# Kernel tuning notes

Measured on AMD Instinct MI355X. Metric: run time of the kernel, lower is better.

The kernel has to match this reference:

```python
import jax, jax.numpy as jnp
import numpy as np

N = 8192
D_IN = 512
HID = 1024
EMB = 64
N_EFF = 2
N_CLASSES = 16
MARGIN = 0.01


def setup_inputs() -> dict:
    key = jax.random.key(0)
    ks = jax.random.split(key, 10)
    data = jax.random.normal(ks[0], (N, D_IN), dtype=jnp.float32)
    labels = jax.random.randint(ks[1], (N,), 0, N_CLASSES).astype(jnp.float32)
    x = jnp.concatenate([labels[:, None], data], axis=1)  # [N, 1+D_IN]

    def lin(k, fan_in, fan_out):
        return jax.random.normal(k, (fan_in, fan_out), dtype=jnp.float32) / np.sqrt(fan_in)

    return {
        "x": x,
        "W1": lin(ks[2], D_IN, HID), "b1": jnp.zeros((HID,), jnp.float32),
        "W2": lin(ks[3], HID, EMB), "b2": jnp.zeros((EMB,), jnp.float32),
        "W3": lin(ks[4], EMB, HID), "b3": jnp.zeros((HID,), jnp.float32),
        "W4": lin(ks[5], HID, D_IN), "b4": jnp.zeros((D_IN,), jnp.float32),
    }


def reference(x, W1, b1, W2, b2, W3, b3, W4, b4):
    labels = x[:, 0]
    data = x[:, 1:]

    # encoder / decoder (tanh MLP autoencoder)
    embedding = jnp.tanh(data @ W1 + b1) @ W2 + b2          # [N, EMB]
    decoded = jnp.tanh(embedding @ W3 + b3) @ W4 + b4       # [N, D_IN]

    conserved = embedding[:, N_EFF:]                        # [N, C]
    n_conserved = conserved.shape[1]

    # labels.expand + unique(return_inverse) on row-replicated labels is
    # equivalent to comparing the labels directly.
    lbl = labels.astype(jnp.int32)
    Y = lbl[:, None] != lbl[None, :]                        # [N, N] bool

    # D_mean[i,j] = mean_d (c_i - c_j)^2, via Gram-matrix algebra (one pass,
    # no [N,N,C] intermediate).
    sq = jnp.sum(conserved * conserved, axis=1)             # [N]
    gram = conserved @ conserved.T                          # [N, N]
    D_mean = jnp.maximum(sq[:, None] + sq[None, :] - 2.0 * gram, 0.0) / n_conserved

    Yf = Y.astype(D_mean.dtype)
    n_diff = jnp.sum(Yf)
    C_sim = jnp.sum(Yf * D_mean) / (n_diff + 1.0)
    C_diff = jnp.sum((1.0 - Yf) * jnp.maximum(0.0, MARGIN - D_mean)) / (
        (D_mean.shape[0] * D_mean.shape[1] - n_diff) + 1.0)

    return decoded, C_sim, C_diff
```

## Files before the change

kernel.cpp:

```cpp
#include <hip/hip_runtime.h>
#include <stdint.h>

#define NROWS 8192
#define DIN   512
#define HIDN  1024
#define EMBN  64
#define NCONS 62
#define NCLS  16
#define MARGINF 0.01f

typedef unsigned short u16;
typedef __attribute__((ext_vector_type(8))) short short8;
typedef __attribute__((ext_vector_type(4))) float floatx4;

__device__ __forceinline__ u16 f32_to_bf16(float f) {
  union { float f; uint32_t u; } x; x.f = f;
  uint32_t u = x.u;
  uint32_t r = (u + 0x7FFFu + ((u >> 16) & 1u)) >> 16;
  return (u16)r;
}

__device__ __forceinline__ float bf16_to_f32(u16 h) {
  union { uint32_t u; float f; } x; x.u = (uint32_t)h << 16;
  return x.f;
}

__device__ __forceinline__ float fast_tanh(float x) {
  float xc = fminf(fmaxf(x, -10.f), 10.f);
  float e = __expf(2.f * xc);
  return (e - 1.f) * __builtin_amdgcn_rcpf(e + 1.f);
}

__device__ __forceinline__ void load_lds16(const u16* g, u16* l) {
  __builtin_amdgcn_global_load_lds(
      (const __attribute__((address_space(1))) void*)g,
      (__attribute__((address_space(3))) void*)l, 16, 0, 0);
}

__device__ __forceinline__ void pack_tile(const float* __restrict__ W,
                                          u16* __restrict__ Wp,
                                          int N, int KU, int t, int lane)
{
  const int r = lane >> 2, slot = lane & 3;
  const int c = slot ^ ((r >> 1) & 3);
  const int nt = t / KU, ku = t - nt * KU;
  const int n = nt * 16 + r;
  const int kb = ku * 32 + c * 8;
  short8 v;
#pragma unroll
  for (int j = 0; j < 8; ++j) v[j] = (short)f32_to_bf16(W[(size_t)(kb + j) * N + n]);
  *(short8*)(Wp + ((size_t)t * 64 + lane) * 8) = v;
}

__global__ __launch_bounds__(256)
void prep_all(const float* __restrict__ x,
              const float* __restrict__ W1, const float* __restrict__ W2,
              const float* __restrict__ W3, const float* __restrict__ W4,
              u16* __restrict__ A0p, u16* __restrict__ W1p,
              u16* __restrict__ W2p, u16* __restrict__ W3p,
              u16* __restrict__ W4p, float* __restrict__ slab,
              int* __restrict__ labels, int* __restrict__ hist32)
{
  __shared__ int hh[NCLS];
  const int b = blockIdx.x;
  const int tid = threadIdx.x;
  const int tl = tid >> 6, lane = tid & 63;
  if (b < 2048) {
    if (b < 32) {
      if (tid < NCLS) hh[tid] = 0;
      const int row = b * 256 + tid;
      const int lab = (int)x[(size_t)row * 513];
      labels[row] = lab;
      __syncthreads();
      atomicAdd(&hh[lab], 1);
      __syncthreads();
      if (tid < NCLS) hist32[b * NCLS + tid] = hh[tid];
    }
    const int t = b * 4 + tl;
    const int rt = t >> 4, ku = t & 15;
    const int r = lane & 15, q = lane >> 4;
    const float* src = x + (size_t)(rt * 16 + r) * 513 + 1 + ku * 32 + q * 8;
    short8 v;
#pragma unroll
    for (int j = 0; j < 8; ++j) v[j] = (short)f32_to_bf16(src[j]);
    *(short8*)(A0p + ((size_t)t * 64 + lane) * 8) = v;
  } else if (b < 2304) {
    pack_tile(W1, W1p, 1024, 16, (b - 2048) * 4 + tl, lane);
  } else if (b < 2336) {
    pack_tile(W2, W2p, 64, 32, (b - 2304) * 4 + tl, lane);
  } else if (b < 2368) {
    pack_tile(W3, W3p, 1024, 2, (b - 2336) * 4 + tl, lane);
  } else if (b < 2624) {
    pack_tile(W4, W4p, 512, 32, (b - 2368) * 4 + tl, lane);
  } else {
    for (int i = tid; i < 4096; i += 256) slab[i] = 0.f;
  }
}

__global__ __launch_bounds__(256)
void gemm12(const u16* __restrict__ A0p, const u16* __restrict__ W1p,
            const float* __restrict__ b1, const u16* __restrict__ W2p,
            float* __restrict__ Ef4,
            const int* __restrict__ labels, const int* __restrict__ hist32,
            int* __restrict__ offs, int* __restrict__ counts,
            int* __restrict__ idx)
{
  __shared__ u16 lB[2][16 * 512];
  __shared__ u16 Hc[4][64 * 66];
  __shared__ int colsum[NCLS], preblk[NCLS], scur[NCLS];

  const int tid = threadIdx.x, wave = tid >> 6, lane = tid & 63;

  if (blockIdx.x >= 128) {
    const int sb = (blockIdx.x - 128) * 4 + blockIdx.y;
    if (tid < NCLS) {
      int s = 0, p = 0;
      for (int b2 = 0; b2 < 32; ++b2) {
        const int h = hist32[b2 * NCLS + tid];
        s += h;
        if (b2 < sb * 2) p += h;
      }
      colsum[tid] = s;
      preblk[tid] = p;
    }
    __syncthreads();
    if (tid < NCLS) {
      int o = 0;
      for (int c = 0; c < tid; ++c) o += colsum[c];
      scur[tid] = o + preblk[tid];
      if (sb == 0) {
        counts[tid] = colsum[tid];
        offs[tid] = o;
        if (tid == NCLS - 1) offs[NCLS] = o + colsum[NCLS - 1];
      }
    }
    __syncthreads();
    for (int i = tid; i < 512; i += 256) {
      const int row = sb * 512 + i;
      const int p = atomicAdd(&scur[labels[row]], 1);
      idx[p] = row;
    }
    return;
  }

  const int quad = lane >> 4, l15 = lane & 15;
  const int wm = wave >> 1, wn = wave & 1;
  const int xslot = (l15 >> 1) & 3;
  const int m0 = blockIdx.x * 64;
  const int g = blockIdx.y;

  floatx4 Hacc[4][2][2];
#pragma unroll
  for (int c = 0; c < 4; ++c)
#pragma unroll
    for (int i = 0; i < 2; ++i)
#pragma unroll
      for (int j = 0; j < 2; ++j) Hacc[c][i][j] = (floatx4){0.f, 0.f, 0.f, 0.f};

#pragma unroll
  for (int u = 0; u < 4; ++u) {
    const int jt = wave + u * 4;
    load_lds16(W1p + (size_t)((g * 16 + jt) * 16) * 512 + lane * 8, lB[0] + jt * 512);
  }
  __syncthreads();

  for (int s = 0; s < 16; ++s) {
    const int p = s & 1;
    if (s < 15) {
#pragma unroll
      for (int u = 0; u < 4; ++u) {
        const int jt = wave + u * 4;
        load_lds16(W1p + (size_t)((g * 16 + jt) * 16 + s + 1) * 512 + lane * 8,
                   lB[1 - p] + jt * 512);
      }
    }
    short8 af[2];
#pragma unroll
    for (int i = 0; i < 2; ++i)
      af[i] = *(const short8*)(A0p +
               (size_t)((blockIdx.x * 4 + wm * 2 + i) * 16 + s) * 512 + lane * 8);
#pragma unroll
    for (int c = 0; c < 4; ++c)
#pragma unroll
      for (int j = 0; j < 2; ++j) {
        const short8 bf = *(const short8*)(lB[p] + (c * 4 + wn * 2 + j) * 512
                              + l15 * 32 + ((quad ^ xslot) << 3));
#pragma unroll
        for (int i = 0; i < 2; ++i)
          Hacc[c][i][j] = __builtin_amdgcn_mfma_f32_16x16x32_bf16(af[i], bf, Hacc[c][i][j], 0, 0, 0);
      }
    __syncthreads();
  }

  u16* lW2 = &lB[0][0];
#pragma unroll
  for (int u = 0; u < 8; ++u) {
    const int t = wave * 8 + u;
    load_lds16(W2p + (size_t)((t >> 3) * 32 + g * 8 + (t & 7)) * 512 + lane * 8,
               lW2 + t * 512);
  }
#pragma unroll
  for (int c = 0; c < 4; ++c)
#pragma unroll
    for (int j = 0; j < 2; ++j) {
      const int col = wn * 32 + j * 16 + l15;
      const float bv = b1[g * 256 + c * 64 + col];
#pragma unroll
      for (int i = 0; i < 2; ++i)
#pragma unroll
        for (int r = 0; r < 4; ++r)
          Hc[c][(wm * 32 + i * 16 + quad * 4 + r) * 66 + col] =
              f32_to_bf16(fast_tanh(Hacc[c][i][j][r] + bv));
    }
  __syncthreads();

  floatx4 Eacc[2][2];
#pragma unroll
  for (int i = 0; i < 2; ++i)
#pragma unroll
    for (int j = 0; j < 2; ++j) Eacc[i][j] = (floatx4){0.f, 0.f, 0.f, 0.f};

#pragma unroll
  for (int es = 0; es < 8; ++es) {
    const int cc = es >> 1, hh2 = es & 1;
    short8 af2[2];
#pragma unroll
    for (int i = 0; i < 2; ++i)
      af2[i] = *(const short8*)(Hc[cc] + (wm * 32 + i * 16 + l15) * 66 + hh2 * 32 + quad * 8);
#pragma unroll
    for (int j = 0; j < 2; ++j) {
      const short8 bf = *(const short8*)(lW2 + ((wn * 2 + j) * 8 + es) * 512
                            + l15 * 32 + ((quad ^ xslot) << 3));
#pragma unroll
      for (int i = 0; i < 2; ++i)
        Eacc[i][j] = __builtin_amdgcn_mfma_f32_16x16x32_bf16(af2[i], bf, Eacc[i][j], 0, 0, 0);
    }
  }

  float* Efg = Ef4 + (size_t)g * NROWS * 64;
#pragma unroll
  for (int i = 0; i < 2; ++i)
#pragma unroll
    for (int j = 0; j < 2; ++j) {
      const int col = wn * 32 + j * 16 + l15;
#pragma unroll
      for (int r = 0; r < 4; ++r) {
        const int row = m0 + wm * 32 + i * 16 + quad * 4 + r;
        Efg[(size_t)row * 64 + col] = Eacc[i][j][r];
      }
    }
}

__global__ __launch_bounds__(256)
void stats3(const float* __restrict__ Ef4, const float* __restrict__ b2,
            const int* __restrict__ labels, const u16* __restrict__ W3p,
            const float* __restrict__ b3,
            u16* __restrict__ Ebf, float* __restrict__ sqrow,
            float* __restrict__ vsum, float* __restrict__ Ssum,
            u16* __restrict__ T)
{
  __shared__ float lv[NCLS][64];
  __shared__ float lsq[NCLS][64];
  __shared__ u16 El[32 * 66];
  const int tid = threadIdx.x;
  for (int i = tid; i < NCLS * 64; i += 256) {
    ((float*)lv)[i] = 0.f; ((float*)lsq)[i] = 0.f;
  }
  __syncthreads();

  const int wave = tid >> 6, lane = tid & 63;
  const float bv = b2[lane];
  const int base0 = blockIdx.x * 32;
  const int base = base0 + wave * 8;
  for (int r = 0; r < 8; ++r) {
    const int row = base + r;
    const int c = labels[row];
    float acc = bv;
#pragma unroll
    for (int g = 0; g < 4; ++g)
      acc += Ef4[((size_t)g * NROWS + row) * 64 + lane];
    const u16 h = f32_to_bf16(acc);
    Ebf[(size_t)row * 64 + lane] = h;
    El[(wave * 8 + r) * 66 + lane] = h;
    float v = bf16_to_f32(h);
    if (lane < 2) v = 0.f;
    const float v2 = v * v;
    atomicAdd(&lv[c][lane], v);
    atomicAdd(&lsq[c][lane], v2);
    float s = v2;
    for (int o = 32; o > 0; o >>= 1) s += __shfl_xor(s, o);
    if (lane == 0) sqrow[row] = s;
  }
  __syncthreads();

  for (int i = tid; i < NCLS * 64; i += 256) {
    const int c = i >> 6, k = i & 63;
    if (k >= 2) atomicAdd(&vsum[c * NCONS + k - 2], lv[c][k]);
  }
  if (tid < NCLS) {
    float s = 0.f;
    for (int k = 0; k < 64; ++k) s += lsq[tid][k];
    atomicAdd(&Ssum[tid], s);
  }

  const int quad = lane >> 4, l15 = lane & 15;
  const int wn = wave;
  const int lamb = l15 * 4 + (quad ^ ((l15 >> 1) & 3));

  floatx4 acc3[2][16];
#pragma unroll
  for (int i = 0; i < 2; ++i)
#pragma unroll
    for (int jj = 0; jj < 16; ++jj) acc3[i][jj] = (floatx4){0.f, 0.f, 0.f, 0.f};

#pragma unroll
  for (int kk = 0; kk < 2; ++kk) {
    short8 af[2];
#pragma unroll
    for (int i = 0; i < 2; ++i)
      af[i] = *(const short8*)(El + (i * 16 + l15) * 66 + kk * 32 + quad * 8);
#pragma unroll
    for (int jj = 0; jj < 16; ++jj) {
      const int nt = wn * 16 + jj;
      const short8 bf = *(const short8*)(W3p + (size_t)(nt * 2 + kk) * 512 + lamb * 8);
#pragma unroll
      for (int i = 0; i < 2; ++i)
        acc3[i][jj] = __builtin_amdgcn_mfma_f32_16x16x32_bf16(af[i], bf, acc3[i][jj], 0, 0, 0);
    }
  }

#pragma unroll
  for (int i = 0; i < 2; ++i)
#pragma unroll
    for (int jj = 0; jj < 16; ++jj) {
      const int col = wn * 256 + jj * 16 + l15;
      const float bv3 = b3[col];
#pragma unroll
      for (int r = 0; r < 4; ++r) {
        const int row = base0 + i * 16 + quad * 4 + r;
        T[(size_t)row * 1024 + col] = f32_to_bf16(fast_tanh(acc3[i][jj][r] + bv3));
      }
    }
}

__global__ __launch_bounds__(256)
void gemm4(const u16* __restrict__ T, const u16* __restrict__ W4p,
           const float* __restrict__ b4, float* __restrict__ out)
{
  __shared__ u16 lA[2][16 * 512];
  __shared__ u16 lB[2][8 * 512];

  const int tid = threadIdx.x, wave = tid >> 6, lane = tid & 63;
  const int quad = lane >> 4, l15 = lane & 15;
  const int wm = wave >> 1, wn = wave & 1;
  const int xslot = (l15 >> 1) & 3;
  const int lin = blockIdx.x + (int)gridDim.x * blockIdx.y;
  const int n0 = (lin >> 6) * 64;
  const int m0 = (lin & 63) * 128;
  const int srow = lane >> 2;
  const int schunk = (lane & 3) ^ ((lane >> 3) & 3);

  auto stage = [&](int s, int buf) {
#pragma unroll
    for (int q = 0; q < 6; ++q) {
      const int u = wave + q * 4;
      if (u < 16) {
        const int rg = u >> 1, kh = u & 1;
        load_lds16(T + (size_t)(m0 + rg * 16 + srow) * 1024 + s * 64 + kh * 32 + schunk * 8,
                   (buf ? lA[1] : lA[0]) + u * 512 + lane * 8);
      } else {
        const int v = u - 16, nt = v >> 1, kh = v & 1;
        load_lds16(W4p + (size_t)(((n0 >> 4) + nt) * 32 + s * 2 + kh) * 512 + lane * 8,
                   (buf ? lB[1] : lB[0]) + v * 512 + lane * 8);
      }
    }
  };

  stage(0, 0);
  __syncthreads();

  floatx4 acc[4][2];
#pragma unroll
  for (int i = 0; i < 4; ++i)
#pragma unroll
    for (int j = 0; j < 2; ++j) acc[i][j] = (floatx4){0.f, 0.f, 0.f, 0.f};

  for (int s = 0; s < 16; ++s) {
    const int p = s & 1;
    if (s < 15) stage(s + 1, 1 - p);
#pragma unroll
    for (int kk = 0; kk < 2; ++kk) {
      short8 af[4], bf[2];
#pragma unroll
      for (int i = 0; i < 4; ++i)
        af[i] = *(const short8*)(lA[p] + ((wm * 4 + i) * 2 + kk) * 512
                                 + l15 * 32 + ((quad ^ xslot) << 3));
#pragma unroll
      for (int j = 0; j < 2; ++j)
        bf[j] = *(const short8*)(lB[p] + ((wn * 2 + j) * 2 + kk) * 512
                                 + l15 * 32 + ((quad ^ xslot) << 3));
#pragma unroll
      for (int i = 0; i < 4; ++i)
#pragma unroll
        for (int j = 0; j < 2; ++j)
          acc[i][j] = __builtin_amdgcn_mfma_f32_16x16x32_bf16(af[i], bf[j], acc[i][j], 0, 0, 0);
    }
    __syncthreads();
  }

#pragma unroll
  for (int i = 0; i < 4; ++i)
#pragma unroll
    for (int j = 0; j < 2; ++j) {
      const int col = n0 + wn * 32 + j * 16 + l15;
      const float bv = b4[col];
#pragma unroll
      for (int r = 0; r < 4; ++r) {
        const int row = m0 + wm * 64 + i * 16 + quad * 4 + r;
        out[(size_t)row * 512 + col] = acc[i][j][r] + bv;
      }
    }
}

__global__ __launch_bounds__(256)
void pairwise_mfma(const u16* __restrict__ Ebf, const float* __restrict__ sqrow,
                   const int* __restrict__ idx, const int* __restrict__ offs,
                   float* __restrict__ pair_sum)
{
  const int cls = blockIdx.y;
  int p = blockIdx.x, ti = 0, cnt = 6;
  while (p >= cnt) { p -= cnt; ++ti; --cnt; }
  const int tj = ti + p;

  const int start = offs[cls];
  const int n = offs[cls + 1] - start;
  if (ti * 128 >= n || tj * 128 >= n) return;

  constexpr int LDA = 66;
  __shared__ u16 Li[128 * LDA];
  __shared__ u16 Lj[128 * LDA];
  __shared__ float sqI[128], sqJ[128];
  __shared__ float red4[4];

  const int tid = threadIdx.x;
  for (int e = tid; e < 2048; e += 256) {
    const int t = e >> 10;
    const int row = (e >> 3) & 127;
    const int ch = e & 7;
    const int g = (t ? tj : ti) * 128 + row;
    short8 v = (short8)0;
    if (g < n) {
      v = *(const short8*)(Ebf + (size_t)idx[start + g] * EMBN + ch * 8);
      if (ch == 0) { v[0] = 0; v[1] = 0; }
    }
    *(short8*)((t ? Lj : Li) + row * LDA + ch * 8) = v;
  }
  {
    const int t = tid >> 7, row = tid & 127;
    const int g = (t ? tj : ti) * 128 + row;
    (t ? sqJ : sqI)[row] = (g < n) ? sqrow[idx[start + g]] : 0.f;
  }
  __syncthreads();

  const int wave = tid >> 6, lane = tid & 63;
  const int wm = wave >> 1, wn = wave & 1;
  const int quad = lane >> 4, l15 = lane & 15;

  floatx4 acc[4][4];
#pragma unroll
  for (int i = 0; i < 4; ++i)
#pragma unroll
    for (int j = 0; j < 4; ++j) acc[i][j] = (floatx4){0.f, 0.f, 0.f, 0.f};

#pragma unroll
  for (int ks = 0; ks < 2; ++ks) {
    short8 af[4], bf[4];
#pragma unroll
    for (int i = 0; i < 4; ++i)
      af[i] = *(const short8*)(Li + (wm * 64 + i * 16 + l15) * LDA + ks * 32 + quad * 8);
#pragma unroll
    for (int j = 0; j < 4; ++j)
      bf[j] = *(const short8*)(Lj + (wn * 64 + j * 16 + l15) * LDA + ks * 32 + quad * 8);
#pragma unroll
    for (int i = 0; i < 4; ++i)
#pragma unroll
      for (int j = 0; j < 4; ++j)
        acc[i][j] = __builtin_amdgcn_mfma_f32_16x16x32_bf16(af[i], bf[j], acc[i][j], 0, 0, 0);
  }

  float local = 0.f;
#pragma unroll
  for (int i = 0; i < 4; ++i)
#pragma unroll
    for (int j = 0; j < 4; ++j)
#pragma unroll
      for (int r = 0; r < 4; ++r) {
        const int row = wm * 64 + i * 16 + quad * 4 + r;
        const int col = wn * 64 + j * 16 + l15;
        const int gi = ti * 128 + row, gj = tj * 128 + col;
        if (gi < n && gj < n && gi != gj) {
          const float D = (sqI[row] + sqJ[col] - 2.f * acc[i][j][r]) * (1.f / 62.f);
          local += fmaxf(0.f, MARGINF - D);
        }
      }
  if (ti < tj) local *= 2.f;

  for (int o = 32; o > 0; o >>= 1) local += __shfl_xor(local, o);
  if (lane == 0) red4[wave] = local;
  __syncthreads();
  if (tid == 0)
    atomicAdd(pair_sum, red4[0] + red4[1] + red4[2] + red4[3]);
}

__device__ __forceinline__ double block_reduce_d(double v, double* red, int tid) {
  red[tid] = v;
  __syncthreads();
  for (int st = 128; st > 0; st >>= 1) {
    if (tid < st) red[tid] += red[tid + st];
    __syncthreads();
  }
  const double r = red[0];
  __syncthreads();
  return r;
}

__global__ __launch_bounds__(256)
void finalize(const float* __restrict__ vsum, const float* __restrict__ Ssum,
              const int* __restrict__ counts, const float* __restrict__ pair_sum,
              float* __restrict__ out2)
{
  const int tid = threadIdx.x;
  __shared__ double red[256];

  double v = 0.0;
  if (tid < NCLS) v = (double)Ssum[tid] * (double)(NROWS - counts[tid]);
  const double t1 = block_reduce_d(v, red, tid);

  v = 0.0;
  if (tid < NCLS) { const double nc = (double)counts[tid]; v = nc * nc; }
  const double n_same = block_reduce_d(v, red, tid);

  v = 0.0;
  for (int i = tid; i < NCLS * NCONS; i += 256) { const double w = vsum[i]; v += w * w; }
  const double t2 = block_reduce_d(v, red, tid);

  v = 0.0;
  if (tid < NCONS) {
    double Vk = 0.0;
    for (int c = 0; c < NCLS; ++c) Vk += (double)vsum[c * NCONS + tid];
    v = Vk * Vk;
  }
  const double t3 = block_reduce_d(v, red, tid);

  if (tid == 0) {
    const double n_diff = (double)NROWS * (double)NROWS - n_same;
    const double sim = 2.0 * t1 - 2.0 * (t3 - t2);
    const double C_sim = sim / 62.0 / (n_diff + 1.0);
    const double C_diff = ((double)pair_sum[0] + (double)NROWS * (double)MARGINF)
                          / (n_same + 1.0);
    out2[0] = (float)C_sim;
    out2[1] = (float)C_diff;
  }
}

extern "C" void kernel_launch(void* const* d_in, const int* in_sizes, int n_in,
                              void* d_out, int out_size, void* d_ws, size_t ws_size,
                              hipStream_t stream)
{
  const float* x  = (const float*)d_in[0];
  const float* W1 = (const float*)d_in[1];
  const float* b1 = (const float*)d_in[2];
  const float* W2 = (const float*)d_in[3];
  const float* b2 = (const float*)d_in[4];
  const float* W3 = (const float*)d_in[5];
  const float* b3 = (const float*)d_in[6];
  const float* W4 = (const float*)d_in[7];
  const float* b4 = (const float*)d_in[8];
  float* out = (float*)d_out;

  char* ws = (char*)d_ws;
  const size_t KB = 1024, MB = 1ull << 20;
  u16* A0p    = (u16*)(ws + 0);
  u16* W1p    = (u16*)(ws + 8 * MB);
  u16* W2p    = (u16*)(ws + 9 * MB);
  u16* W3p    = (u16*)(ws + 9 * MB + 128 * KB);
  u16* W4p    = (u16*)(ws + 9 * MB + 256 * KB);
  float* Ef4  = (float*)(ws + 10 * MB + 256 * KB);
  u16* Ebf    = (u16*)(ws + 18 * MB + 256 * KB);
  int* labels = (int*)(ws + 19 * MB + 256 * KB);
  int* idx    = (int*)(ws + 19 * MB + 288 * KB);
  float* slab = (float*)(ws + 19 * MB + 320 * KB);
  int*   counts  = (int*)slab;
  int*   offs    = counts + 16;
  float* Ssum    = (float*)(counts + 96);
  float* psum    = (float*)(counts + 128);
  float* vsum    = (float*)(counts + 256);
  float* sqrow = (float*)(ws + 19 * MB + 336 * KB);
  int* hist32 = (int*)(ws + 19 * MB + 368 * KB);
  u16* T      = (u16*)(ws + 20 * MB);
  (void)in_sizes; (void)n_in; (void)out_size; (void)ws_size;

  prep_all<<<dim3(2625), dim3(256), 0, stream>>>(x, W1, W2, W3, W4,
                                                 A0p, W1p, W2p, W3p, W4p,
                                                 slab, labels, hist32);
  gemm12<<<dim3(132, 4), dim3(256), 0, stream>>>(A0p, W1p, b1, W2p, Ef4,
                                                 labels, hist32, offs, counts, idx);
  stats3<<<dim3(256), dim3(256), 0, stream>>>(Ef4, b2, labels, W3p, b3,
                                              Ebf, sqrow, vsum, Ssum, T);
  gemm4<<<dim3(8, 64), dim3(256), 0, stream>>>(T, W4p, b4, out);
  pairwise_mfma<<<dim3(21, 16), dim3(256), 0, stream>>>(Ebf, sqrow, idx, offs, psum);
  finalize<<<dim3(1), dim3(256), 0, stream>>>(vsum, Ssum, counts, psum,
                                              out + (size_t)NROWS * DIN);
}
```

Baseline: 174.7 us.

## Merge gemm4 and pairwise kernels into one launch; replicate stats atomics

Combines the final decoder GEMM and the class-pairwise Gram kernel into a single 'tail' launch that splits blocks by index and shares one LDS buffer, so the two independent stages can run concurrently on the GPU and one launch is removed. Separately, the per-class vsum/Ssum atomics in stats3 are spread across 16 replicas to cut contention, and finalize now reduces those replicas. The shared LDS union raises per-block LDS use for the pairwise blocks, and prep_all zeroes a larger slab.

```diff
diff --git a/kernel.cpp b/kernel.cpp
--- a/kernel.cpp
+++ b/kernel.cpp
@@ -8,6 +8,7 @@
 #define NCONS 62
 #define NCLS  16
 #define MARGINF 0.01f
+#define NREP  16
 
 typedef unsigned short u16;
 typedef __attribute__((ext_vector_type(8))) short short8;
@@ -93,7 +94,8 @@
   } else if (b < 2624) {
     pack_tile(W4, W4p, 512, 32, (b - 2368) * 4 + tl, lane);
   } else {
-    for (int i = tid; i < 4096; i += 256) slab[i] = 0.f;
+    float* dst = slab + (size_t)(b - 2624) * 4096;
+    for (int i = tid; i < 4096; i += 256) dst[i] = 0.f;
   }
 }
 
@@ -256,7 +258,7 @@
             const int* __restrict__ labels, const u16* __restrict__ W3p,
             const float* __restrict__ b3,
             u16* __restrict__ Ebf, float* __restrict__ sqrow,
-            float* __restrict__ vsum, float* __restrict__ Ssum,
+            float* __restrict__ vsumR, float* __restrict__ SsumR,
             u16* __restrict__ T)
 {
   __shared__ float lv[NCLS][64];
@@ -268,6 +270,7 @@
   }
   __syncthreads();
 
+  const int rep = blockIdx.x & (NREP - 1);
   const int wave = tid >> 6, lane = tid & 63;
   const float bv = b2[lane];
   const int base0 = blockIdx.x * 32;
@@ -295,12 +298,12 @@
 
   for (int i = tid; i < NCLS * 64; i += 256) {
     const int c = i >> 6, k = i & 63;
-    if (k >= 2) atomicAdd(&vsum[c * NCONS + k - 2], lv[c][k]);
+    if (k >= 2) atomicAdd(&vsumR[rep * (NCLS * NCONS) + c * NCONS + k - 2], lv[c][k]);
   }
   if (tid < NCLS) {
     float s = 0.f;
     for (int k = 0; k < 64; ++k) s += lsq[tid][k];
-    atomicAdd(&Ssum[tid], s);
+    atomicAdd(&SsumR[rep * NCLS + tid], s);
   }
 
   const int quad = lane >> 4, l15 = lane & 15;
@@ -344,91 +347,93 @@
 }
 
 __global__ __launch_bounds__(256)
-void gemm4(const u16* __restrict__ T, const u16* __restrict__ W4p,
-           const float* __restrict__ b4, float* __restrict__ out)
+void tail(const u16* __restrict__ T, const u16* __restrict__ W4p,
+          const float* __restrict__ b4, float* __restrict__ out,
+          const u16* __restrict__ Ebf, const float* __restrict__ sqrow,
+          const int* __restrict__ idx, const int* __restrict__ offs,
+          float* __restrict__ pair_sum)
 {
-  __shared__ u16 lA[2][16 * 512];
-  __shared__ u16 lB[2][8 * 512];
-
+  __shared__ u16 uni[24576];
   const int tid = threadIdx.x, wave = tid >> 6, lane = tid & 63;
   const int quad = lane >> 4, l15 = lane & 15;
-  const int wm = wave >> 1, wn = wave & 1;
-  const int xslot = (l15 >> 1) & 3;
-  const int lin = blockIdx.x + (int)gridDim.x * blockIdx.y;
-  const int n0 = (lin >> 6) * 64;
-  const int m0 = (lin & 63) * 128;
-  const int srow = lane >> 2;
-  const int schunk = (lane & 3) ^ ((lane >> 3) & 3);
-
-  auto stage = [&](int s, int buf) {
-#pragma unroll
-    for (int q = 0; q < 6; ++q) {
-      const int u = wave + q * 4;
-      if (u < 16) {
-        const int rg = u >> 1, kh = u & 1;
-        load_lds16(T + (size_t)(m0 + rg * 16 + srow) * 1024 + s * 64 + kh * 32 + schunk * 8,
-                   (buf ? lA[1] : lA[0]) + u * 512 + lane * 8);
-      } else {
-        const int v = u - 16, nt = v >> 1, kh = v & 1;
-        load_lds16(W4p + (size_t)(((n0 >> 4) + nt) * 32 + s * 2 + kh) * 512 + lane * 8,
-                   (buf ? lB[1] : lB[0]) + v * 512 + lane * 8);
-      }
-    }
-  };
-
-  stage(0, 0);
-  __syncthreads();
-
-  floatx4 acc[4][2];
-#pragma unroll
-  for (int i = 0; i < 4; ++i)
-#pragma unroll
-    for (int j = 0; j < 2; ++j) acc[i][j] = (floatx4){0.f, 0.f, 0.f, 0.f};
-
-  for (int s = 0; s < 16; ++s) {
-    const int p = s & 1;
-    if (s < 15) stage(s + 1, 1 - p);
-#pragma unroll
-    for (int kk = 0; kk < 2; ++kk) {
-      short8 af[4], bf[2];
-#pragma unroll
-      for (int i = 0; i < 4; ++i)
-        af[i] = *(const short8*)(lA[p] + ((wm * 4 + i) * 2 + kk) * 512
-                                 + l15 * 32 + ((quad ^ xslot) << 3));
-#pragma unroll
-      for (int j = 0; j < 2; ++j)
-        bf[j] = *(const short8*)(lB[p] + ((wn * 2 + j) * 2 + kk) * 512
-                                 + l15 * 32 + ((quad ^ xslot) << 3));
-#pragma unroll
-      for (int i = 0; i < 4; ++i)
+
+  if (blockIdx.x < 512) {
+    u16* lA = uni;
+    u16* lBb = uni + 16384;
+    const int wm = wave >> 1, wn = wave & 1;
+    const int xslot = (l15 >> 1) & 3;
+    const int lin = blockIdx.x;
+    const int n0 = (lin >> 6) * 64;
+    const int m0 = (lin & 63) * 128;
+    const int srow = lane >> 2;
+    const int schunk = (lane & 3) ^ ((lane >> 3) & 3);
+
+    auto stage = [&](int s, int buf) {
+#pragma unroll
+      for (int q = 0; q < 6; ++q) {
+        const int u = wave + q * 4;
+        if (u < 16) {
+          const int rg = u >> 1, kh = u & 1;
+          load_lds16(T + (size_t)(m0 + rg * 16 + srow) * 1024 + s * 64 + kh * 32 + schunk * 8,
+                     lA + buf * 8192 + u * 512 + lane * 8);
+        } else {
+          const int v = u - 16, nt = v >> 1, kh = v & 1;
+          load_lds16(W4p + (size_t)(((n0 >> 4) + nt) * 32 + s * 2 + kh) * 512 + lane * 8,
+                     lBb + buf * 4096 + v * 512 + lane * 8);
+        }
+      }
+    };
+
+    stage(0, 0);
+    __syncthreads();
+
+    floatx4 acc[4][2];
+#pragma unroll
+    for (int i = 0; i < 4; ++i)
+#pragma unroll
+      for (int j = 0; j < 2; ++j) acc[i][j] = (floatx4){0.f, 0.f, 0.f, 0.f};
+
+    for (int s = 0; s < 16; ++s) {
+      const int p = s & 1;
+      if (s < 15) stage(s + 1, 1 - p);
+#pragma unroll
+      for (int kk = 0; kk < 2; ++kk) {
+        short8 af[4], bf[2];
+#pragma unroll
+        for (int i = 0; i < 4; ++i)
+          af[i] = *(const short8*)(lA + p * 8192 + ((wm * 4 + i) * 2 + kk) * 512
+                                   + l15 * 32 + ((quad ^ xslot) << 3));
 #pragma unroll
         for (int j = 0; j < 2; ++j)
-          acc[i][j] = __builtin_amdgcn_mfma_f32_16x16x32_bf16(af[i], bf[j], acc[i][j], 0, 0, 0);
-    }
-    __syncthreads();
-  }
-
-#pragma unroll
-  for (int i = 0; i < 4; ++i)
-#pragma unroll
-    for (int j = 0; j < 2; ++j) {
-      const int col = n0 + wn * 32 + j * 16 + l15;
-      const float bv = b4[col];
-#pragma unroll
-      for (int r = 0; r < 4; ++r) {
-        const int row = m0 + wm * 64 + i * 16 + quad * 4 + r;
-        out[(size_t)row * 512 + col] = acc[i][j][r] + bv;
-      }
-    }
-}
-
-__global__ __launch_bounds__(256)
-void pairwise_mfma(const u16* __restrict__ Ebf, const float* __restrict__ sqrow,
-                   const int* __restrict__ idx, const int* __restrict__ offs,
-                   float* __restrict__ pair_sum)
-{
-  const int cls = blockIdx.y;
-  int p = blockIdx.x, ti = 0, cnt = 6;
+          bf[j] = *(const short8*)(lBb + p * 4096 + ((wn * 2 + j) * 2 + kk) * 512
+                                   + l15 * 32 + ((quad ^ xslot) << 3));
+#pragma unroll
+        for (int i = 0; i < 4; ++i)
+#pragma unroll
+          for (int j = 0; j < 2; ++j)
+            acc[i][j] = __builtin_amdgcn_mfma_f32_16x16x32_bf16(af[i], bf[j], acc[i][j], 0, 0, 0);
+      }
+      __syncthreads();
+    }
+
+#pragma unroll
+    for (int i = 0; i < 4; ++i)
+#pragma unroll
+      for (int j = 0; j < 2; ++j) {
+        const int col = n0 + wn * 32 + j * 16 + l15;
+        const float bv = b4[col];
+#pragma unroll
+        for (int r = 0; r < 4; ++r) {
+          const int row = m0 + wm * 64 + i * 16 + quad * 4 + r;
+          out[(size_t)row * 512 + col] = acc[i][j][r] + bv;
+        }
+      }
+    return;
+  }
+
+  const int q = blockIdx.x - 512;
+  const int cls = q / 21;
+  int p = q - cls * 21, ti = 0, cnt = 6;
   while (p >= cnt) { p -= cnt; ++ti; --cnt; }
   const int tj = ti + p;
 
@@ -437,12 +442,12 @@
   if (ti * 128 >= n || tj * 128 >= n) return;
 
   constexpr int LDA = 66;
-  __shared__ u16 Li[128 * LDA];
-  __shared__ u16 Lj[128 * LDA];
-  __shared__ float sqI[128], sqJ[128];
-  __shared__ float red4[4];
-
-  const int tid = threadIdx.x;
+  u16* Li = uni;
+  u16* Lj = uni + 128 * LDA;
+  float* sqI = (float*)(uni + 2 * 128 * LDA);
+  float* sqJ = sqI + 128;
+  float* red4 = sqJ + 128;
+
   for (int e = tid; e < 2048; e += 256) {
     const int t = e >> 10;
     const int row = (e >> 3) & 127;
@@ -462,9 +467,7 @@
   }
   __syncthreads();
 
-  const int wave = tid >> 6, lane = tid & 63;
   const int wm = wave >> 1, wn = wave & 1;
-  const int quad = lane >> 4, l15 = lane & 15;
 
   floatx4 acc[4][4];
 #pragma unroll
@@ -525,15 +528,27 @@
 }
 
 __global__ __launch_bounds__(256)
-void finalize(const float* __restrict__ vsum, const float* __restrict__ Ssum,
+void finalize(const float* __restrict__ vsumR, const float* __restrict__ SsumR,
               const int* __restrict__ counts, const float* __restrict__ pair_sum,
               float* __restrict__ out2)
 {
   const int tid = threadIdx.x;
   __shared__ double red[256];
+  __shared__ float vtot[NCLS * NCONS];
+
+  for (int i = tid; i < NCLS * NCONS; i += 256) {
+    float s = 0.f;
+    for (int r = 0; r < NREP; ++r) s += vsumR[r * (NCLS * NCONS) + i];
+    vtot[i] = s;
+  }
+  __syncthreads();
 
   double v = 0.0;
-  if (tid < NCLS) v = (double)Ssum[tid] * (double)(NROWS - counts[tid]);
+  if (tid < NCLS) {
+    float Sc = 0.f;
+    for (int r = 0; r < NREP; ++r) Sc += SsumR[r * NCLS + tid];
+    v = (double)Sc * (double)(NROWS - counts[tid]);
+  }
   const double t1 = block_reduce_d(v, red, tid);
 
   v = 0.0;
@@ -541,13 +556,13 @@
   const double n_same = block_reduce_d(v, red, tid);
 
   v = 0.0;
-  for (int i = tid; i < NCLS * NCONS; i += 256) { const double w = vsum[i]; v += w * w; }
+  for (int i = tid; i < NCLS * NCONS; i += 256) { const double w = vtot[i]; v += w * w; }
   const double t2 = block_reduce_d(v, red, tid);
 
   v = 0.0;
   if (tid < NCONS) {
     double Vk = 0.0;
-    for (int c = 0; c < NCLS; ++c) Vk += (double)vsum[c * NCONS + tid];
+    for (int c = 0; c < NCLS; ++c) Vk += (double)vtot[c * NCONS + tid];
     v = Vk * Vk;
   }
   const double t3 = block_reduce_d(v, red, tid);
@@ -589,26 +604,26 @@
   u16* Ebf    = (u16*)(ws + 18 * MB + 256 * KB);
   int* labels = (int*)(ws + 19 * MB + 256 * KB);
   int* idx    = (int*)(ws + 19 * MB + 288 * KB);
-  float* slab = (float*)(ws + 19 * MB + 320 * KB);
+  float* sqrow = (float*)(ws + 19 * MB + 320 * KB);
+  int* hist32 = (int*)(ws + 19 * MB + 352 * KB);
+  float* slab = (float*)(ws + 19 * MB + 384 * KB);
   int*   counts  = (int*)slab;
   int*   offs    = counts + 16;
-  float* Ssum    = (float*)(counts + 96);
-  float* psum    = (float*)(counts + 128);
-  float* vsum    = (float*)(counts + 256);
-  float* sqrow = (float*)(ws + 19 * MB + 336 * KB);
-  int* hist32 = (int*)(ws + 19 * MB + 368 * KB);
+  float* psum    = slab + 64;
+  float* SsumR   = slab + 128;
+  float* vsumR   = slab + 512;
   u16* T      = (u16*)(ws + 20 * MB);
   (void)in_sizes; (void)n_in; (void)out_size; (void)ws_size;
 
-  prep_all<<<dim3(2625), dim3(256), 0, stream>>>(x, W1, W2, W3, W4,
+  prep_all<<<dim3(2630), dim3(256), 0, stream>>>(x, W1, W2, W3, W4,
                                                  A0p, W1p, W2p, W3p, W4p,
                                                  slab, labels, hist32);
   gemm12<<<dim3(132, 4), dim3(256), 0, stream>>>(A0p, W1p, b1, W2p, Ef4,
                                                  labels, hist32, offs, counts, idx);
   stats3<<<dim3(256), dim3(256), 0, stream>>>(Ef4, b2, labels, W3p, b3,
-                                              Ebf, sqrow, vsum, Ssum, T);
-  gemm4<<<dim3(8, 64), dim3(256), 0, stream>>>(T, W4p, b4, out);
-  pairwise_mfma<<<dim3(21, 16), dim3(256), 0, stream>>>(Ebf, sqrow, idx, offs, psum);
-  finalize<<<dim3(1), dim3(256), 0, stream>>>(vsum, Ssum, counts, psum,
+                                              Ebf, sqrow, vsumR, SsumR, T);
+  tail<<<dim3(848), dim3(256), 0, stream>>>(T, W4p, b4, out,
+                                            Ebf, sqrow, idx, offs, psum);
+  finalize<<<dim3(1), dim3(256), 0, stream>>>(vsumR, SsumR, counts, psum,
                                               out + (size_t)NROWS * DIN);
 }
```

Measured after the change: 172.2 us. Within noise of the previous version (-1.4%).
